# Kernel optimization log

Measured on AMD Instinct MI355X. Metric: run time of the kernel, lower is better.

Reference implementation:

```python
import jax, jax.numpy as jnp
import numpy as np

EPS = 1e-12  # matches torch F.normalize eps clamp


def _l2norm(v, axis):
    n = jnp.sqrt(jnp.sum(v * v, axis=axis, keepdims=True))
    return v / jnp.maximum(n, EPS)


def setup_inputs() -> dict:
    key = jax.random.key(0)
    k1, k2, k3, k4 = jax.random.split(key, 4)
    N, C, H, W, K = 64, 128, 64, 64, 64
    x = jax.random.normal(k1, (N, C, H, W), dtype=jnp.float32)
    conv_w = jax.random.normal(k2, (K, C), dtype=jnp.float32) * 0.1  # 1x1 conv weight squeezed
    conv_b = jax.random.normal(k3, (K,), dtype=jnp.float32) * 0.1
    centroids = jax.random.uniform(k4, (K, C), dtype=jnp.float32)
    return {"x": x, "conv_w": conv_w, "conv_b": conv_b, "centroids": centroids}


def reference(x, conv_w, conv_b, centroids):
    N, C = x.shape[:2]
    K = centroids.shape[0]
    xf = x.reshape(N, C, -1)                                   # (N, C, P) with P = H*W
    # 1x1 conv == per-pixel linear map over channels
    logits = jnp.einsum('ncp,kc->nkp', xf, conv_w) + conv_b[None, :, None]
    a = jax.nn.softmax(logits, axis=1)                         # soft assignment over clusters
    # vlad[n,k,c] = sum_p a[n,k,p] * (x[n,c,p] - centroids[k,c])
    vlad = jnp.einsum('nkp,ncp->nkc', a, xf) \
        - jnp.sum(a, axis=-1)[:, :, None] * centroids[None]    # (N, K, C)
    vlad = _l2norm(vlad, axis=2)                               # intra-cluster normalization
    vlad = vlad.reshape(N, K * C)
    return _l2norm(vlad, axis=1)
```

## Files before the change

kernel.cpp:

```cpp
#include <hip/hip_runtime.h>
#include <math.h>

#define NNIMG 64
#define CCH 128
#define KK 64
#define PP 4096
#define BSPLIT 8
#define PB (PP / BSPLIT)
#define PC 64
#define NCHUNK (PB / PC)

typedef __attribute__((ext_vector_type(8))) short short8;
typedef __attribute__((ext_vector_type(4))) float f32x4;

__device__ __forceinline__ unsigned short bf16_hi(float f) {
  unsigned u = __float_as_uint(f);
  unsigned r = u + 0x7FFFu + ((u >> 16) & 1u);
  return (unsigned short)(r >> 16);
}
__device__ __forceinline__ float bf16_tof(unsigned short h) {
  return __uint_as_float(((unsigned)h) << 16);
}
__device__ __forceinline__ unsigned pack_hl(float f) {
  unsigned u = __float_as_uint(f);
  unsigned r = u + 0x7FFFu + ((u >> 16) & 1u);
  float hf = __uint_as_float(r & 0xFFFF0000u);
  unsigned lo = __float_as_uint(f - hf);
  return __builtin_amdgcn_perm(lo, r, 0x07060302u);
}

__device__ __forceinline__ void lgkm_barrier() {
  __asm__ volatile("s_waitcnt lgkmcnt(0)\n\ts_barrier" ::: "memory");
}
__device__ __forceinline__ void vm_barrier() {
  __asm__ volatile("s_waitcnt vmcnt(0)\n\ts_barrier" ::: "memory");
}

__device__ __forceinline__ void load_to_lds16(const float* g, float* l) {
  __builtin_amdgcn_global_load_lds((const __attribute__((address_space(1))) void*)g,
                                   (__attribute__((address_space(3))) void*)l, 16, 0, 0);
}

__global__ __launch_bounds__(256, 2) void netvlad_main(
    const float* __restrict__ x, const float* __restrict__ conv_w,
    const float* __restrict__ conv_b, float* __restrict__ vlad_part,
    float* __restrict__ asum_part) {
  __shared__ __align__(16) float xraw[CCH * PC];
  __shared__ __align__(16) unsigned int pc_hl[PC * 132];
  __shared__ __align__(16) unsigned short a_lds[KK * 72];
  __shared__ float b_lds[KK];
  __shared__ float asum_buf[4 * KK];

  const int t = threadIdx.x;
  const int lane = t & 63;
  const int wv = t >> 6;
  const int m = lane & 15;
  const int q = lane >> 4;

  const int n = blockIdx.x / BSPLIT;
  const int blk = blockIdx.x % BSPLIT;
  const float* xbase = x + (size_t)n * CCH * PP + blk * PB;

  auto issue_dma = [&](int ch) {
#pragma unroll
    for (int i = 0; i < 8; ++i) {
      int row = 8 * wv + i;
      const float* g =
          xbase + (size_t)(4 * row + (lane >> 4)) * PP + ch * PC + (lane & 15) * 4;
      load_to_lds16(g, &xraw[row * 256]);
    }
  };

  issue_dma(0);

  if (t < KK) b_lds[t] = conv_b[t];

  short8 Whi[4][4], Wlo[4][4];
#pragma unroll
  for (int kt = 0; kt < 4; ++kt) {
#pragma unroll
    for (int cs = 0; cs < 4; ++cs) {
      const float* wp = conv_w + (kt * 16 + m) * CCH + cs * 32 + q * 8;
      float4 wa = *(const float4*)wp;
      float4 wb = *(const float4*)(wp + 4);
      float fv[8] = {wa.x, wa.y, wa.z, wa.w, wb.x, wb.y, wb.z, wb.w};
      short8 h, l;
#pragma unroll
      for (int j = 0; j < 8; ++j) {
        unsigned short hb = bf16_hi(fv[j]);
        h[j] = (short)hb;
        l[j] = (short)bf16_hi(fv[j] - bf16_tof(hb));
      }
      Whi[kt][cs] = h;
      Wlo[kt][cs] = l;
    }
  }

  f32x4 vacc[4][2];
#pragma unroll
  for (int kt = 0; kt < 4; ++kt)
#pragma unroll
    for (int ct = 0; ct < 2; ++ct) vacc[kt][ct] = (f32x4){0.f, 0.f, 0.f, 0.f};
  float asum_acc[16];
#pragma unroll
  for (int i = 0; i < 16; ++i) asum_acc[i] = 0.f;

  const int crow = t >> 3;
  const int pr = t & 7;
  const int prow = wv * 16 + m;
  const int swz_r = 8 * ((prow >> 2) & 3);

#pragma unroll 1
  for (int ch = 0; ch < NCHUNK; ++ch) {
    vm_barrier();

#pragma unroll
    for (int ci = 0; ci < 4; ++ci) {
      int c = crow + ci * 32;
      int cc = c ^ (8 * (pr & 3));
#pragma unroll
      for (int rep = 0; rep < 2; ++rep) {
        int pl = pr * 4 + rep * 32;
        float4 v = *(const float4*)&xraw[c * 64 + pl];
        float fv[4] = {v.x, v.y, v.z, v.w};
#pragma unroll
        for (int j = 0; j < 4; ++j) pc_hl[(pl + j) * 132 + cc] = pack_hl(fv[j]);
      }
    }
    lgkm_barrier();

    if (ch < NCHUNK - 1) issue_dma(ch + 1);

    f32x4 acc1[4];
#pragma unroll
    for (int kt = 0; kt < 4; ++kt) acc1[kt] = (f32x4){0.f, 0.f, 0.f, 0.f};
    const unsigned int* pcrow = pc_hl + prow * 132;
#pragma unroll
    for (int cs = 0; cs < 4; ++cs) {
      int base = cs * 32 + ((q << 3) ^ swz_r);
      uint4 s0 = *(const uint4*)&pcrow[base];
      uint4 s1 = *(const uint4*)&pcrow[base + 4];
      unsigned int ss[8] = {s0.x, s0.y, s0.z, s0.w, s1.x, s1.y, s1.z, s1.w};
      unsigned int hs[4], ls[4];
#pragma unroll
      for (int i = 0; i < 4; ++i) {
        hs[i] = __builtin_amdgcn_perm(ss[2 * i + 1], ss[2 * i], 0x05040100u);
        ls[i] = __builtin_amdgcn_perm(ss[2 * i + 1], ss[2 * i], 0x07060302u);
      }
      short8 Bh, Bl;
      __builtin_memcpy(&Bh, hs, 16);
      __builtin_memcpy(&Bl, ls, 16);
#pragma unroll
      for (int kt = 0; kt < 4; ++kt) {
        acc1[kt] = __builtin_amdgcn_mfma_f32_16x16x32_bf16(Whi[kt][cs], Bh, acc1[kt], 0, 0, 0);
        acc1[kt] = __builtin_amdgcn_mfma_f32_16x16x32_bf16(Whi[kt][cs], Bl, acc1[kt], 0, 0, 0);
        acc1[kt] = __builtin_amdgcn_mfma_f32_16x16x32_bf16(Wlo[kt][cs], Bh, acc1[kt], 0, 0, 0);
      }
    }

    float ssum = 0.f;
#pragma unroll
    for (int kt = 0; kt < 4; ++kt)
#pragma unroll
      for (int r = 0; r < 4; ++r) {
        float e = __expf(acc1[kt][r] + b_lds[kt * 16 + q * 4 + r]);
        acc1[kt][r] = e;
        ssum += e;
      }
    ssum += __shfl_xor(ssum, 16, 64);
    ssum += __shfl_xor(ssum, 32, 64);
    float inv = 1.0f / ssum;
#pragma unroll
    for (int kt = 0; kt < 4; ++kt)
#pragma unroll
      for (int r = 0; r < 4; ++r) {
        float a = acc1[kt][r] * inv;
        asum_acc[kt * 4 + r] += a;
        a_lds[(kt * 16 + q * 4 + r) * 72 + prow] = bf16_hi(a);
      }
    lgkm_barrier();

#pragma unroll
    for (int ps = 0; ps < 2; ++ps) {
      short8 Af[4];
#pragma unroll
      for (int kt = 0; kt < 4; ++kt)
        Af[kt] = *(const short8*)&a_lds[(kt * 16 + m) * 72 + ps * 32 + q * 8];
#pragma unroll
      for (int ct = 0; ct < 2; ++ct) {
        int c = wv * 32 + ct * 16 + m;
        unsigned int g[8];
#pragma unroll
        for (int j = 0; j < 8; ++j) {
          int p = ps * 32 + q * 8 + j;
          g[j] = pc_hl[p * 132 + (c ^ (8 * ((p >> 2) & 3)))];
        }
        unsigned int hs[4];
#pragma unroll
        for (int i = 0; i < 4; ++i)
          hs[i] = __builtin_amdgcn_perm(g[2 * i + 1], g[2 * i], 0x05040100u);
        short8 Bf;
        __builtin_memcpy(&Bf, hs, 16);
#pragma unroll
        for (int kt = 0; kt < 4; ++kt)
          vacc[kt][ct] = __builtin_amdgcn_mfma_f32_16x16x32_bf16(Af[kt], Bf, vacc[kt][ct], 0, 0, 0);
      }
    }
  }

  float* vt = (float*)pc_hl;
#pragma unroll
  for (int kt = 0; kt < 4; ++kt)
#pragma unroll
    for (int ct = 0; ct < 2; ++ct)
#pragma unroll
      for (int r = 0; r < 4; ++r)
        vt[(kt * 16 + q * 4 + r) * 132 + wv * 32 + ct * 16 + m] = vacc[kt][ct][r];
#pragma unroll
  for (int i = 0; i < 16; ++i) {
    float v = asum_acc[i];
    v += __shfl_xor(v, 1, 64);
    v += __shfl_xor(v, 2, 64);
    v += __shfl_xor(v, 4, 64);
    v += __shfl_xor(v, 8, 64);
    if (m == 0) asum_buf[wv * 64 + (i >> 2) * 16 + q * 4 + (i & 3)] = v;
  }
  lgkm_barrier();
  {
    const int k = t >> 2, c0 = (t & 3) * 32;
    const size_t ob = (size_t)blockIdx.x * (KK * CCH) + k * CCH + c0;
#pragma unroll
    for (int i = 0; i < 8; ++i)
      *(float4*)&vlad_part[ob + i * 4] = *(const float4*)&vt[k * 132 + c0 + i * 4];
  }
  if (t < 64) {
    float s = asum_buf[t] + asum_buf[64 + t] + asum_buf[128 + t] + asum_buf[192 + t];
    asum_part[blockIdx.x * 64 + t] = s;
  }
}

__global__ __launch_bounds__(256) void netvlad_finish(
    const float* __restrict__ vlad_part, const float* __restrict__ asum_part,
    const float* __restrict__ centroids, float* __restrict__ out) {
  const int t = threadIdx.x;
  const int w = t >> 6, ln = t & 63;
  const int idx = blockIdx.x * 4 + w;
  const int n = idx >> 6, k = idx & 63;
  const int c = ln * 2;
  float v0 = 0.f, v1 = 0.f;
#pragma unroll
  for (int b = 0; b < BSPLIT; ++b) {
    float2 pv = *(const float2*)&vlad_part[(size_t)(n * BSPLIT + b) * (KK * CCH) + k * CCH + c];
    v0 += pv.x;
    v1 += pv.y;
  }
  float s = 0.f;
#pragma unroll
  for (int b = 0; b < BSPLIT; ++b) s += asum_part[(n * BSPLIT + b) * KK + k];
  float2 ce = *(const float2*)&centroids[k * CCH + c];
  v0 -= s * ce.x;
  v1 -= s * ce.y;
  float ssq = v0 * v0 + v1 * v1;
#pragma unroll
  for (int off = 32; off > 0; off >>= 1) ssq += __shfl_xor(ssq, off, 64);
  float inv = 0.125f / fmaxf(sqrtf(ssq), 1e-12f);
  float2 o;
  o.x = v0 * inv;
  o.y = v1 * inv;
  *(float2*)&out[(size_t)n * (KK * CCH) + k * CCH + c] = o;
}

extern "C" void kernel_launch(void* const* d_in, const int* in_sizes, int n_in,
                              void* d_out, int out_size, void* d_ws, size_t ws_size,
                              hipStream_t stream) {
  const float* x = (const float*)d_in[0];
  const float* conv_w = (const float*)d_in[1];
  const float* conv_b = (const float*)d_in[2];
  const float* centroids = (const float*)d_in[3];
  float* out = (float*)d_out;

  float* vlad_part = (float*)d_ws;
  float* asum_part = vlad_part + (size_t)NNIMG * BSPLIT * KK * CCH;

  netvlad_main<<<NNIMG * BSPLIT, 256, 0, stream>>>(x, conv_w, conv_b, vlad_part, asum_part);
  netvlad_finish<<<NNIMG * KK / 4, 256, 0, stream>>>(vlad_part, asum_part, centroids, out);
}
```

Baseline: 237.8 us.

## Drop split-bf16 logits, halve block size, reduce partials via atomics

Replaces the three-pass hi/lo bf16 emulation of the logits GEMM with a single bf16 MFMA, using truncated bf16 packs of x stored in LDS. Blocks shrink to 128 threads with 32-pixel chunks and twice as many pixel splits. Per-block partial VLAD and assignment sums are reduced with global atomicAdd into a zeroed buffer instead of being written out and summed in the finish kernel. The bias is folded into the accumulator init. The aim is fewer MFMAs and less partial-buffer traffic, at the cost of lower logit precision and atomic contention plus an extra memset.

After: 229.4 us. -3.5%, faster.

```diff
diff --git a/kernel.cpp b/kernel.cpp
--- a/kernel.cpp
+++ b/kernel.cpp
@@ -5,15 +5,15 @@
 #define CCH 128
 #define KK 64
 #define PP 4096
-#define BSPLIT 8
+#define BSPLIT 16
 #define PB (PP / BSPLIT)
-#define PC 64
+#define PC 32
 #define NCHUNK (PB / PC)
 
 typedef __attribute__((ext_vector_type(8))) short short8;
 typedef __attribute__((ext_vector_type(4))) float f32x4;
 
-__device__ __forceinline__ unsigned short bf16_hi(float f) {
+__device__ __forceinline__ unsigned short bf16_rtne(float f) {
   unsigned u = __float_as_uint(f);
   unsigned r = u + 0x7FFFu + ((u >> 16) & 1u);
   return (unsigned short)(r >> 16);
@@ -21,19 +21,12 @@
 __device__ __forceinline__ float bf16_tof(unsigned short h) {
   return __uint_as_float(((unsigned)h) << 16);
 }
-__device__ __forceinline__ unsigned pack_hl(float f) {
-  unsigned u = __float_as_uint(f);
-  unsigned r = u + 0x7FFFu + ((u >> 16) & 1u);
-  float hf = __uint_as_float(r & 0xFFFF0000u);
-  unsigned lo = __float_as_uint(f - hf);
-  return __builtin_amdgcn_perm(lo, r, 0x07060302u);
-}
 
 __device__ __forceinline__ void lgkm_barrier() {
   __asm__ volatile("s_waitcnt lgkmcnt(0)\n\ts_barrier" ::: "memory");
 }
 __device__ __forceinline__ void vm_barrier() {
-  __asm__ volatile("s_waitcnt vmcnt(0)\n\ts_barrier" ::: "memory");
+  __asm__ volatile("s_waitcnt vmcnt(0) lgkmcnt(0)\n\ts_barrier" ::: "memory");
 }
 
 __device__ __forceinline__ void load_to_lds16(const float* g, float* l) {
@@ -41,15 +34,14 @@
                                    (__attribute__((address_space(3))) void*)l, 16, 0, 0);
 }
 
-__global__ __launch_bounds__(256, 2) void netvlad_main(
+__global__ __launch_bounds__(128, 2) void netvlad_main(
     const float* __restrict__ x, const float* __restrict__ conv_w,
-    const float* __restrict__ conv_b, float* __restrict__ vlad_part,
-    float* __restrict__ asum_part) {
+    const float* __restrict__ conv_b, float* __restrict__ vg,
+    float* __restrict__ ag) {
   __shared__ __align__(16) float xraw[CCH * PC];
-  __shared__ __align__(16) unsigned int pc_hl[PC * 132];
-  __shared__ __align__(16) unsigned short a_lds[KK * 72];
-  __shared__ float b_lds[KK];
-  __shared__ float asum_buf[4 * KK];
+  __shared__ __align__(16) unsigned int pc[PC * 66];
+  __shared__ __align__(16) unsigned short a_lds[KK * 40];
+  __shared__ float asum_buf[2 * KK];
 
   const int t = threadIdx.x;
   const int lane = t & 63;
@@ -57,74 +49,71 @@
   const int m = lane & 15;
   const int q = lane >> 4;
 
-  const int n = blockIdx.x / BSPLIT;
-  const int blk = blockIdx.x % BSPLIT;
+  const int n = blockIdx.x >> 4;
+  const int blk = blockIdx.x & 15;
   const float* xbase = x + (size_t)n * CCH * PP + blk * PB;
 
+  const int dma_c = (lane >> 3);
+  const int dma_p = (lane & 7) * 4;
   auto issue_dma = [&](int ch) {
 #pragma unroll
     for (int i = 0; i < 8; ++i) {
-      int row = 8 * wv + i;
-      const float* g =
-          xbase + (size_t)(4 * row + (lane >> 4)) * PP + ch * PC + (lane & 15) * 4;
-      load_to_lds16(g, &xraw[row * 256]);
+      int rowbase = wv * 64 + i * 8;
+      const float* g = xbase + (size_t)(rowbase + dma_c) * PP + ch * PC + dma_p;
+      load_to_lds16(g, &xraw[rowbase * PC]);
     }
   };
 
   issue_dma(0);
 
-  if (t < KK) b_lds[t] = conv_b[t];
-
-  short8 Whi[4][4], Wlo[4][4];
-#pragma unroll
-  for (int kt = 0; kt < 4; ++kt) {
+  short8 Whi[4][4];
+#pragma unroll
+  for (int kt = 0; kt < 4; ++kt)
 #pragma unroll
     for (int cs = 0; cs < 4; ++cs) {
       const float* wp = conv_w + (kt * 16 + m) * CCH + cs * 32 + q * 8;
       float4 wa = *(const float4*)wp;
       float4 wb = *(const float4*)(wp + 4);
       float fv[8] = {wa.x, wa.y, wa.z, wa.w, wb.x, wb.y, wb.z, wb.w};
-      short8 h, l;
-#pragma unroll
-      for (int j = 0; j < 8; ++j) {
-        unsigned short hb = bf16_hi(fv[j]);
-        h[j] = (short)hb;
-        l[j] = (short)bf16_hi(fv[j] - bf16_tof(hb));
-      }
+      short8 h;
+#pragma unroll
+      for (int j = 0; j < 8; ++j) h[j] = (short)bf16_rtne(fv[j]);
       Whi[kt][cs] = h;
-      Wlo[kt][cs] = l;
-    }
-  }
-
-  f32x4 vacc[4][2];
-#pragma unroll
-  for (int kt = 0; kt < 4; ++kt)
-#pragma unroll
-    for (int ct = 0; ct < 2; ++ct) vacc[kt][ct] = (f32x4){0.f, 0.f, 0.f, 0.f};
+    }
+  float b_regs[4][4];
+#pragma unroll
+  for (int kt = 0; kt < 4; ++kt)
+#pragma unroll
+    for (int r = 0; r < 4; ++r) b_regs[kt][r] = conv_b[kt * 16 + q * 4 + r];
+
+  f32x4 vacc[4][4];
+#pragma unroll
+  for (int kt = 0; kt < 4; ++kt)
+#pragma unroll
+    for (int ct = 0; ct < 4; ++ct) vacc[kt][ct] = (f32x4){0.f, 0.f, 0.f, 0.f};
   float asum_acc[16];
 #pragma unroll
   for (int i = 0; i < 16; ++i) asum_acc[i] = 0.f;
 
-  const int crow = t >> 3;
-  const int pr = t & 7;
+  const int sp = lane & 31;
+  const int sh = lane >> 5;
   const int prow = wv * 16 + m;
-  const int swz_r = 8 * ((prow >> 2) & 3);
+  const unsigned sel_hi = 0x07060302u;
+  const unsigned sel_g2 = (m & 1) ? 0x07060302u : 0x05040100u;
 
 #pragma unroll 1
   for (int ch = 0; ch < NCHUNK; ++ch) {
     vm_barrier();
 
-#pragma unroll
-    for (int ci = 0; ci < 4; ++ci) {
-      int c = crow + ci * 32;
-      int cc = c ^ (8 * (pr & 3));
-#pragma unroll
-      for (int rep = 0; rep < 2; ++rep) {
-        int pl = pr * 4 + rep * 32;
-        float4 v = *(const float4*)&xraw[c * 64 + pl];
-        float fv[4] = {v.x, v.y, v.z, v.w};
-#pragma unroll
-        for (int j = 0; j < 4; ++j) pc_hl[(pl + j) * 132 + cc] = pack_hl(fv[j]);
+    {
+      const float* xr = xraw + (4 * wv + 2 * sh) * PC + sp;
+      const int pbase = sp * 66 + 2 * wv + sh;
+#pragma unroll
+      for (int i = 0; i < 16; ++i) {
+        float x0 = xr[i * (8 * PC)];
+        float x1 = xr[i * (8 * PC) + PC];
+        pc[pbase + 4 * i] =
+            __builtin_amdgcn_perm(__float_as_uint(x1), __float_as_uint(x0), sel_hi);
       }
     }
     lgkm_barrier();
@@ -133,29 +122,19 @@
 
     f32x4 acc1[4];
 #pragma unroll
-    for (int kt = 0; kt < 4; ++kt) acc1[kt] = (f32x4){0.f, 0.f, 0.f, 0.f};
-    const unsigned int* pcrow = pc_hl + prow * 132;
+    for (int kt = 0; kt < 4; ++kt)
+      acc1[kt] = (f32x4){b_regs[kt][0], b_regs[kt][1], b_regs[kt][2], b_regs[kt][3]};
+    const unsigned int* pcrow = pc + prow * 66;
 #pragma unroll
     for (int cs = 0; cs < 4; ++cs) {
-      int base = cs * 32 + ((q << 3) ^ swz_r);
-      uint4 s0 = *(const uint4*)&pcrow[base];
-      uint4 s1 = *(const uint4*)&pcrow[base + 4];
-      unsigned int ss[8] = {s0.x, s0.y, s0.z, s0.w, s1.x, s1.y, s1.z, s1.w};
-      unsigned int hs[4], ls[4];
-#pragma unroll
-      for (int i = 0; i < 4; ++i) {
-        hs[i] = __builtin_amdgcn_perm(ss[2 * i + 1], ss[2 * i], 0x05040100u);
-        ls[i] = __builtin_amdgcn_perm(ss[2 * i + 1], ss[2 * i], 0x07060302u);
-      }
-      short8 Bh, Bl;
-      __builtin_memcpy(&Bh, hs, 16);
-      __builtin_memcpy(&Bl, ls, 16);
-#pragma unroll
-      for (int kt = 0; kt < 4; ++kt) {
-        acc1[kt] = __builtin_amdgcn_mfma_f32_16x16x32_bf16(Whi[kt][cs], Bh, acc1[kt], 0, 0, 0);
-        acc1[kt] = __builtin_amdgcn_mfma_f32_16x16x32_bf16(Whi[kt][cs], Bl, acc1[kt], 0, 0, 0);
-        acc1[kt] = __builtin_amdgcn_mfma_f32_16x16x32_bf16(Wlo[kt][cs], Bh, acc1[kt], 0, 0, 0);
-      }
+      uint2 u01 = *(const uint2*)&pcrow[16 * cs + 4 * q];
+      uint2 u23 = *(const uint2*)&pcrow[16 * cs + 4 * q + 2];
+      unsigned hs[4] = {u01.x, u01.y, u23.x, u23.y};
+      short8 Bf;
+      __builtin_memcpy(&Bf, hs, 16);
+#pragma unroll
+      for (int kt = 0; kt < 4; ++kt)
+        acc1[kt] = __builtin_amdgcn_mfma_f32_16x16x32_bf16(Whi[kt][cs], Bf, acc1[kt], 0, 0, 0);
     }
 
     float ssum = 0.f;
@@ -163,7 +142,7 @@
     for (int kt = 0; kt < 4; ++kt)
 #pragma unroll
       for (int r = 0; r < 4; ++r) {
-        float e = __expf(acc1[kt][r] + b_lds[kt * 16 + q * 4 + r]);
+        float e = __expf(acc1[kt][r]);
         acc1[kt][r] = e;
         ssum += e;
       }
@@ -175,47 +154,43 @@
 #pragma unroll
       for (int r = 0; r < 4; ++r) {
         float a = acc1[kt][r] * inv;
-        asum_acc[kt * 4 + r] += a;
-        a_lds[(kt * 16 + q * 4 + r) * 72 + prow] = bf16_hi(a);
+        unsigned short h = bf16_rtne(a);
+        asum_acc[kt * 4 + r] += bf16_tof(h);
+        a_lds[(kt * 16 + q * 4 + r) * 40 + prow] = h;
       }
     lgkm_barrier();
 
-#pragma unroll
-    for (int ps = 0; ps < 2; ++ps) {
-      short8 Af[4];
+    short8 Af[4];
+#pragma unroll
+    for (int kt = 0; kt < 4; ++kt)
+      Af[kt] = *(const short8*)&a_lds[(kt * 16 + m) * 40 + q * 8];
+#pragma unroll
+    for (int ct = 0; ct < 4; ++ct) {
+      const int ebase = wv * 32 + ct * 8 + (m >> 1);
+      unsigned g[8];
+#pragma unroll
+      for (int j = 0; j < 8; ++j) g[j] = pc[(q * 8 + j) * 66 + ebase];
+      unsigned hs[4];
+#pragma unroll
+      for (int i = 0; i < 4; ++i)
+        hs[i] = __builtin_amdgcn_perm(g[2 * i + 1], g[2 * i], sel_g2);
+      short8 Bf;
+      __builtin_memcpy(&Bf, hs, 16);
 #pragma unroll
       for (int kt = 0; kt < 4; ++kt)
-        Af[kt] = *(const short8*)&a_lds[(kt * 16 + m) * 72 + ps * 32 + q * 8];
-#pragma unroll
-      for (int ct = 0; ct < 2; ++ct) {
-        int c = wv * 32 + ct * 16 + m;
-        unsigned int g[8];
-#pragma unroll
-        for (int j = 0; j < 8; ++j) {
-          int p = ps * 32 + q * 8 + j;
-          g[j] = pc_hl[p * 132 + (c ^ (8 * ((p >> 2) & 3)))];
-        }
-        unsigned int hs[4];
-#pragma unroll
-        for (int i = 0; i < 4; ++i)
-          hs[i] = __builtin_amdgcn_perm(g[2 * i + 1], g[2 * i], 0x05040100u);
-        short8 Bf;
-        __builtin_memcpy(&Bf, hs, 16);
-#pragma unroll
-        for (int kt = 0; kt < 4; ++kt)
-          vacc[kt][ct] = __builtin_amdgcn_mfma_f32_16x16x32_bf16(Af[kt], Bf, vacc[kt][ct], 0, 0, 0);
-      }
+        vacc[kt][ct] = __builtin_amdgcn_mfma_f32_16x16x32_bf16(Af[kt], Bf, vacc[kt][ct], 0, 0, 0);
     }
   }
 
-  float* vt = (float*)pc_hl;
-#pragma unroll
-  for (int kt = 0; kt < 4; ++kt)
-#pragma unroll
-    for (int ct = 0; ct < 2; ++ct)
+  float* vrow = vg + (size_t)n * (KK * CCH);
+#pragma unroll
+  for (int kt = 0; kt < 4; ++kt)
+#pragma unroll
+    for (int ct = 0; ct < 4; ++ct)
 #pragma unroll
       for (int r = 0; r < 4; ++r)
-        vt[(kt * 16 + q * 4 + r) * 132 + wv * 32 + ct * 16 + m] = vacc[kt][ct][r];
+        atomicAdd(&vrow[(kt * 16 + q * 4 + r) * CCH + wv * 64 + ct * 16 + m],
+                  vacc[kt][ct][r]);
 #pragma unroll
   for (int i = 0; i < 16; ++i) {
     float v = asum_acc[i];
@@ -226,40 +201,22 @@
     if (m == 0) asum_buf[wv * 64 + (i >> 2) * 16 + q * 4 + (i & 3)] = v;
   }
   lgkm_barrier();
-  {
-    const int k = t >> 2, c0 = (t & 3) * 32;
-    const size_t ob = (size_t)blockIdx.x * (KK * CCH) + k * CCH + c0;
-#pragma unroll
-    for (int i = 0; i < 8; ++i)
-      *(float4*)&vlad_part[ob + i * 4] = *(const float4*)&vt[k * 132 + c0 + i * 4];
-  }
-  if (t < 64) {
-    float s = asum_buf[t] + asum_buf[64 + t] + asum_buf[128 + t] + asum_buf[192 + t];
-    asum_part[blockIdx.x * 64 + t] = s;
-  }
+  if (t < KK) atomicAdd(&ag[n * KK + t], asum_buf[t] + asum_buf[KK + t]);
 }
 
 __global__ __launch_bounds__(256) void netvlad_finish(
-    const float* __restrict__ vlad_part, const float* __restrict__ asum_part,
+    const float* __restrict__ vg, const float* __restrict__ ag,
     const float* __restrict__ centroids, float* __restrict__ out) {
   const int t = threadIdx.x;
   const int w = t >> 6, ln = t & 63;
   const int idx = blockIdx.x * 4 + w;
   const int n = idx >> 6, k = idx & 63;
   const int c = ln * 2;
-  float v0 = 0.f, v1 = 0.f;
-#pragma unroll
-  for (int b = 0; b < BSPLIT; ++b) {
-    float2 pv = *(const float2*)&vlad_part[(size_t)(n * BSPLIT + b) * (KK * CCH) + k * CCH + c];
-    v0 += pv.x;
-    v1 += pv.y;
-  }
-  float s = 0.f;
-#pragma unroll
-  for (int b = 0; b < BSPLIT; ++b) s += asum_part[(n * BSPLIT + b) * KK + k];
+  float2 v = *(const float2*)&vg[(size_t)(n * KK + k) * CCH + c];
+  float s = ag[n * KK + k];
   float2 ce = *(const float2*)&centroids[k * CCH + c];
-  v0 -= s * ce.x;
-  v1 -= s * ce.y;
+  float v0 = v.x - s * ce.x;
+  float v1 = v.y - s * ce.y;
   float ssq = v0 * v0 + v1 * v1;
 #pragma unroll
   for (int off = 32; off > 0; off >>= 1) ssq += __shfl_xor(ssq, off, 64);
@@ -279,9 +236,11 @@
   const float* centroids = (const float*)d_in[3];
   float* out = (float*)d_out;
 
-  float* vlad_part = (float*)d_ws;
-  float* asum_part = vlad_part + (size_t)NNIMG * BSPLIT * KK * CCH;
-
-  netvlad_main<<<NNIMG * BSPLIT, 256, 0, stream>>>(x, conv_w, conv_b, vlad_part, asum_part);
-  netvlad_finish<<<NNIMG * KK / 4, 256, 0, stream>>>(vlad_part, asum_part, centroids, out);
-}
+  float* vg = (float*)d_ws;
+  float* ag = vg + (size_t)NNIMG * KK * CCH;
+  const size_t zbytes = ((size_t)NNIMG * KK * CCH + NNIMG * KK) * sizeof(float);
+
+  hipMemsetAsync(d_ws, 0, zbytes, stream);
+  netvlad_main<<<NNIMG * BSPLIT, 128, 0, stream>>>(x, conv_w, conv_b, vg, ag);
+  netvlad_finish<<<NNIMG * KK / 4, 256, 0, stream>>>(vg, ag, centroids, out);
+}
```
